# Kernel optimization log

Measured on AMD Instinct MI355X. Metric: run time of the kernel, lower is better.

## Reference

```python
import jax, jax.numpy as jnp
import numpy as np

B, C1, H, W = 2, 128, 64, 64
C_ = C1 // 2


def _conv2d(x, w, b, pad, dil):
    out = jax.lax.conv_general_dilated(
        x, w, (1, 1), [(pad, pad), (pad, pad)], rhs_dilation=(dil, dil),
        dimension_numbers=('NCHW', 'OIHW', 'NCHW'))
    return out + b[None, :, None, None]


def _deform_dw(x, off_w, off_b, w, k, pad, dil):
    # Depthwise DeformConv2d (v1, no modulation), offset_groups=1, stride=1.
    Bn, C, Hn, Wn = x.shape
    K = k * k
    offsets = _conv2d(x, off_w, off_b, pad, dil)          # [B, 2K, H, W]
    off = offsets.reshape(Bn, K, 2, Hn, Wn)               # (dy, dx) per kernel pt
    ky = jnp.repeat(jnp.arange(k) * dil, k).astype(x.dtype)   # [K]
    kx = jnp.tile(jnp.arange(k) * dil, k).astype(x.dtype)     # [K]
    py = off[:, :, 0] + (jnp.arange(Hn, dtype=x.dtype)[:, None] - pad) + ky[None, :, None, None]
    px = off[:, :, 1] + (jnp.arange(Wn, dtype=x.dtype)[None, :] - pad) + kx[None, :, None, None]
    y0 = jnp.floor(py); x0 = jnp.floor(px)
    ly = py - y0; lx = px - x0
    y0i = y0.astype(jnp.int32); x0i = x0.astype(jnp.int32)
    xf = x.reshape(Bn, C, Hn * Wn)

    def corner(yi, xi, wgt):
        valid = (yi >= 0) & (yi < Hn) & (xi >= 0) & (xi < Wn)
        idx = (jnp.clip(yi, 0, Hn - 1) * Wn + jnp.clip(xi, 0, Wn - 1)).reshape(Bn, -1)
        v = jax.vmap(lambda xb, ib: xb[:, ib])(xf, idx).reshape(Bn, C, K, Hn, Wn)
        return v * (wgt * valid.astype(x.dtype))[:, None]

    val = (corner(y0i, x0i, (1 - ly) * (1 - lx))
           + corner(y0i, x0i + 1, (1 - ly) * lx)
           + corner(y0i + 1, x0i, ly * (1 - lx))
           + corner(y0i + 1, x0i + 1, ly * lx))      # [B, C, K, H, W]
    return jnp.einsum('bckhw,ck->bchw', val, w.reshape(C, K))


def _forward(x, cv0_off_w, cv0_off_b, cv0_w, cvs_off_w, cvs_off_b, cvs_w,
             c0_off_w, c0_off_b, c0_w, cs_off_w, cs_off_b, cs_w,
             conv1_w, conv1_b, conv2_w, conv2_b):
    c = x.shape[1] // 2
    y0, y1 = x[:, :c], x[:, c:]
    a0 = _deform_dw(y0, cv0_off_w, cv0_off_b, cv0_w, 3, 1, 1)
    a0 = _deform_dw(a0, cvs_off_w, cvs_off_b, cvs_w, 5, 6, 3)
    a0 = _conv2d(a0, conv1_w, conv1_b, 0, 1)
    a1 = _deform_dw(y1, c0_off_w, c0_off_b, c0_w, 5, 2, 1)
    a1 = _deform_dw(a1, cs_off_w, cs_off_b, cs_w, 7, 9, 3)
    a1 = _conv2d(a1, conv2_w, conv2_b, 0, 1)
    return x * jnp.concatenate([a0, a1], axis=1)


def setup_inputs() -> dict:
    key = jax.random.key(0)
    ks = jax.random.split(key, 18)
    n = lambda k, sh, s: jax.random.normal(k, sh, dtype=jnp.float32) * s
    return {
        'x': n(ks[0], (B, C1, H, W), 1.0),
        'cv0_off_w': n(ks[1], (18, C_, 3, 3), 0.05),  'cv0_off_b': n(ks[2], (18,), 0.05),
        'cv0_w': n(ks[3], (C_, 1, 3, 3), 0.1),
        'cvs_off_w': n(ks[4], (50, C_, 5, 5), 0.05),  'cvs_off_b': n(ks[5], (50,), 0.05),
        'cvs_w': n(ks[6], (C_, 1, 5, 5), 0.1),
        'c0_off_w': n(ks[7], (50, C_, 5, 5), 0.05),   'c0_off_b': n(ks[8], (50,), 0.05),
        'c0_w': n(ks[9], (C_, 1, 5, 5), 0.1),
        'cs_off_w': n(ks[10], (98, C_, 7, 7), 0.05),  'cs_off_b': n(ks[11], (98,), 0.05),
        'cs_w': n(ks[12], (C_, 1, 7, 7), 0.1),
        'conv1_w': n(ks[13], (C_, C_, 1, 1), 0.1),    'conv1_b': n(ks[14], (C_,), 0.05),
        'conv2_w': n(ks[15], (C_, C_, 1, 1), 0.1),    'conv2_b': n(ks[16], (C_,), 0.05),
    }


def reference(x, cv0_off_w, cv0_off_b, cv0_w, cvs_off_w, cvs_off_b, cvs_w,
              c0_off_w, c0_off_b, c0_w, cs_off_w, cs_off_b, cs_w,
              conv1_w, conv1_b, conv2_w, conv2_b):
    return _forward(x, cv0_off_w, cv0_off_b, cv0_w, cvs_off_w, cvs_off_b, cvs_w,
                    c0_off_w, c0_off_b, c0_w, cs_off_w, cs_off_b, cs_w,
                    conv1_w, conv1_b, conv2_w, conv2_b)
```

## Files before the change

kernel.cpp:

```cpp
#include <hip/hip_runtime.h>
#include <hip/hip_bf16.h>

#define HW   4096

typedef __bf16 bf_t;
typedef __bf16 bf8_t __attribute__((ext_vector_type(8)));
typedef float  f4_t  __attribute__((ext_vector_type(4)));
typedef int    i4_t  __attribute__((ext_vector_type(4)));

#define OFF_A    0
#define OFF_B    409600
#define A1_F32   1212416
#define B1_F32   1736704
#define A2_F32   2260992
#define B2_F32   2785280
#define XA_F32   3309568
#define XB_F32   3833856
#define XA_HI    4358144
#define XA_LO    4620288
#define XB_HI    4882432
#define XB_LO    5144576
#define A1_HI    5406720
#define A1_LO    5668864
#define B1_HI    5931008
#define B1_LO    6193152
#define AW_A1    6455296
#define AW_B1    6464512
#define AW_A2    6515712
#define AW_B2    6566912
#define DW_A1    6767616
#define DW_B1    6768192
#define DW_A2    6769792
#define DW_B2    6771392
#define WS_TOT   6774528

__device__ __align__(16) float g_ws[WS_TOT];

__device__ __forceinline__ bf8_t bf8_zero() {
    bf8_t v;
#pragma unroll
    for (int j = 0; j < 8; ++j) v[j] = (bf_t)0.f;
    return v;
}

__device__ __forceinline__ void prep_wA_dev(const float* wg, int aw_off,
                                            int Cout, int K, int NCOT, int lb) {
    const int KK = K * K;
    const int total = KK * NCOT * 128;
    const int idx = lb * 256 + threadIdx.x;
    if (idx >= total) return;
    bf_t* aw = (bf_t*)(g_ws + aw_off);
    int lane = idx & 63;
    int kh   = (idx >> 6) & 1;
    int cot  = (idx >> 7) % NCOT;
    int tap  = idx / (128 * NCOT);
    int co   = cot * 16 + (lane & 15);
    int ci0  = kh * 32 + (lane >> 4) * 8;
    bf8_t v;
#pragma unroll
    for (int j = 0; j < 8; ++j) {
        float f = (co < Cout) ? wg[(co * 64 + ci0 + j) * KK + tap] : 0.f;
        v[j] = (bf_t)f;
    }
    *(bf8_t*)&aw[(long)idx * 8] = v;
}

__device__ __forceinline__ void prep_dwT_dev(const float* w, int dst_off,
                                             int KK, int lb) {
    const int idx = lb * 256 + threadIdx.x;
    if (idx < KK * 64) {
        int c = idx & 63, kk = idx >> 6;
        g_ws[dst_off + kk * 64 + c] = w[c * KK + kk];
    }
}

__global__ __launch_bounds__(256) void prep_split_kernel(
    const float* __restrict__ x,
    const float* cv0_off_w, const float* c0_off_w,
    const float* cvs_off_w, const float* cs_off_w,
    const float* cv0_w, const float* c0_w,
    const float* cvs_w, const float* cs_w)
{
    __shared__ float lds[16 * 68];
    const int bi = blockIdx.x;
    if (bi < 335) {
        if      (bi < 9)   prep_wA_dev(cv0_off_w, AW_A1, 18, 3, 2, bi);
        else if (bi < 59)  prep_wA_dev(c0_off_w,  AW_B1, 50, 5, 4, bi - 9);
        else if (bi < 109) prep_wA_dev(cvs_off_w, AW_A2, 50, 5, 4, bi - 59);
        else if (bi < 305) prep_wA_dev(cs_off_w,  AW_B2, 98, 7, 8, bi - 109);
        else if (bi < 308) prep_dwT_dev(cv0_w, DW_A1, 9,  bi - 305);
        else if (bi < 315) prep_dwT_dev(c0_w,  DW_B1, 25, bi - 308);
        else if (bi < 322) prep_dwT_dev(cvs_w, DW_A2, 25, bi - 315);
        else               prep_dwT_dev(cs_w,  DW_B2, 49, bi - 322);
        return;
    }
    const int s  = bi - 335;
    const int b  = s & 1;
    const int br = (s >> 1) & 1;
    const int p0 = (s >> 2) * 16;
    const float* sb = x + (long)b * (128 * HW) + (long)br * (64 * HW);
    bf_t*  dhi = (bf_t*)(g_ws + (br ? XB_HI : XA_HI));
    bf_t*  dlo = (bf_t*)(g_ws + (br ? XB_LO : XA_LO));
    float* df  = g_ws + (br ? XB_F32 : XA_F32);
    const int t = threadIdx.x;
    {
        const int px = t & 15;
        const int c0 = t >> 4;
#pragma unroll
        for (int pass = 0; pass < 4; ++pass) {
            int ci = c0 + pass * 16;
            lds[px * 68 + ci] = sb[ci * HW + p0 + px];
        }
    }
    __syncthreads();
    if (t < 128) {
        int px = t >> 3, q = t & 7;
        bf8_t vh, vl;
        f4_t  f0, f1;
#pragma unroll
        for (int j = 0; j < 8; ++j) {
            float a = lds[px * 68 + q * 8 + j];
            bf_t hcast = (bf_t)a;
            vh[j] = hcast;
            vl[j] = (bf_t)(a - (float)hcast);
            if (j < 4) f0[j] = a; else f1[j - 4] = a;
        }
        long base = (((long)b * 4096 + p0 + px) * 64) + q * 8;
        *(bf8_t*)&dhi[base] = vh;
        *(bf8_t*)&dlo[base] = vl;
        *(f4_t*)&df[base]     = f0;
        *(f4_t*)&df[base + 4] = f1;
    }
}

template<int K, int DIL, int PAD, int NCOT, int CPG>
__device__ __forceinline__ void mfma_conv_dev(
    int bx, int by, bf_t* smem,
    int hi_off, int lo_off, int aw_off, const float* __restrict__ bias,
    int dst_off, int Cout)
{
    constexpr int COLS = 64 + 2 * PAD;
    const bf_t* shi = (const bf_t*)(g_ws + hi_off);
    const bf_t* slo = (const bf_t*)(g_ws + lo_off);
    const bf_t* aw  = (const bf_t*)(g_ws + aw_off);
    float* dst = g_ws + dst_off;
    bf_t* lds0 = smem;
    bf_t* lds1 = smem + COLS * 72;

    const int t    = threadIdx.x;
    const int lane = t & 63;
    const int wv   = t >> 6;
    const int b    = bx >> 6;
    const int h    = bx & 63;
    const int ct0  = by * CPG;

    const int n0 = lane & 15;
    const int kq = lane >> 4;

    f4_t acc[CPG];
#pragma unroll
    for (int i = 0; i < CPG; ++i) acc[i] = (f4_t){0.f, 0.f, 0.f, 0.f};

    for (int ky = 0; ky < K; ++ky) {
        const int ih = h - PAD + ky * DIL;
        __syncthreads();
        if ((unsigned)ih < 64u) {
            const long rowb = ((long)b * 4096 + ih * 64) * 64;
            for (int c = t; c < COLS * 8; c += 256) {
                int col = c >> 3, q = c & 7;
                int iw = col - PAD;
                bf8_t vh, vl;
                if ((unsigned)iw < 64u) {
                    vh = *(const bf8_t*)&shi[rowb + iw * 64 + q * 8];
                    vl = *(const bf8_t*)&slo[rowb + iw * 64 + q * 8];
                } else { vh = bf8_zero(); vl = bf8_zero(); }
                *(bf8_t*)&lds0[col * 72 + q * 8] = vh;
                *(bf8_t*)&lds1[col * 72 + q * 8] = vl;
            }
        } else {
            bf8_t z = bf8_zero();
            for (int c = t; c < COLS * 8; c += 256) {
                int col = c >> 3, q = c & 7;
                *(bf8_t*)&lds0[col * 72 + q * 8] = z;
                *(bf8_t*)&lds1[col * 72 + q * 8] = z;
            }
        }
        __syncthreads();
#pragma unroll
        for (int kx = 0; kx < K; ++kx) {
            const int tap = ky * K + kx;
            bf8_t afr[CPG][2];
#pragma unroll
            for (int ct = 0; ct < CPG; ++ct)
#pragma unroll
                for (int kh = 0; kh < 2; ++kh)
                    afr[ct][kh] = *(const bf8_t*)
                        &aw[((((long)tap * NCOT + ct0 + ct) * 2 + kh) * 64 + lane) * 8];
            const int colb = (wv * 16 + n0 + kx * DIL) * 72;
#pragma unroll
            for (int kh = 0; kh < 2; ++kh) {
                const bf8_t bh = *(const bf8_t*)&lds0[colb + kh * 32 + kq * 8];
                const bf8_t bl = *(const bf8_t*)&lds1[colb + kh * 32 + kq * 8];
#pragma unroll
                for (int ct = 0; ct < CPG; ++ct) {
                    acc[ct] = __builtin_amdgcn_mfma_f32_16x16x32_bf16(
                        afr[ct][kh], bh, acc[ct], 0, 0, 0);
                    acc[ct] = __builtin_amdgcn_mfma_f32_16x16x32_bf16(
                        afr[ct][kh], bl, acc[ct], 0, 0, 0);
                }
            }
        }
    }

    const int w = wv * 16 + n0;
#pragma unroll
    for (int ct = 0; ct < CPG; ++ct) {
#pragma unroll
        for (int r = 0; r < 4; ++r) {
            int co = (ct0 + ct) * 16 + kq * 4 + r;
            if (co < Cout)
                dst[((long)b * Cout + co) * HW + h * 64 + w] = acc[ct][r] + bias[co];
        }
    }
}

__global__ __launch_bounds__(256) void conv_s1_kernel(
    const float* __restrict__ biasA, const float* __restrict__ biasB)
{
    extern __shared__ __align__(16) bf_t smem1[];
    const int bi = blockIdx.x;
    const int g = bi / 3, r = bi % 3;
    if (r == 0)
        mfma_conv_dev<3, 1, 1, 2, 1>(g & 127, g >> 7, smem1,
                                     XA_HI, XA_LO, AW_A1, biasA, OFF_A, 18);
    else {
        const int s = 2 * g + (r - 1);
        mfma_conv_dev<5, 1, 2, 4, 1>(s & 127, s >> 7, smem1,
                                     XB_HI, XB_LO, AW_B1, biasB, OFF_B, 50);
    }
}

__global__ __launch_bounds__(256) void conv_s2_kernel(
    const float* __restrict__ biasA, const float* __restrict__ biasB)
{
    extern __shared__ __align__(16) bf_t smem2[];
    const int bi = blockIdx.x;
    const int s = bi >> 1;
    if ((bi & 1) == 0)
        mfma_conv_dev<5, 3, 6, 4, 1>(s & 127, s >> 7, smem2,
                                     A1_HI, A1_LO, AW_A2, biasA, OFF_A, 50);
    else
        mfma_conv_dev<7, 3, 9, 8, 2>(s & 127, s >> 7, smem2,
                                     B1_HI, B1_LO, AW_B2, biasB, OFF_B, 98);
}

template<int KK, int WRITE_HILO>
__device__ __forceinline__ void sample_fused_dev(
    int bx, float* recs, int src_off, int off_off, int dwt_off,
    int dst_off, int hi_off, int lo_off, int K, int pad, int dil)
{
    const int t   = threadIdx.x;
    const int pgi = ((bx & 7) << 8) | (bx >> 3);

    for (int rec = t; rec < 4 * KK; rec += 256) {
        const int wv = rec & 3;
        const int kk = rec >> 2;
        const int pg = pgi * 4 + wv;
        const int b  = pg >> 12;
        const int p  = pg & 4095;
        const int h  = p >> 6, w = p & 63;
        const float oy = g_ws[off_off + ((long)(b * 2 * KK + 2 * kk)) * HW + p];
        const float ox = g_ws[off_off + ((long)(b * 2 * KK + 2 * kk + 1)) * HW + p];
        const float py = oy + (float)(h - pad + (kk / K) * dil);
        const float px = ox + (float)(w - pad + (kk % K) * dil);
        const float fy = floorf(py), fx = floorf(px);
        const float ly = py - fy,    lx = px - fx;
        const int y0 = (int)fy, x0 = (int)fx;
        const int y1 = y0 + 1,  x1 = x0 + 1;
        const float vy0 = ((unsigned)y0 < 64u) ? 1.f : 0.f;
        const float vy1 = ((unsigned)y1 < 64u) ? 1.f : 0.f;
        const float vx0 = ((unsigned)x0 < 64u) ? 1.f : 0.f;
        const float vx1 = ((unsigned)x1 < 64u) ? 1.f : 0.f;
        const float w00 = (1.f - ly) * (1.f - lx) * vy0 * vx0;
        const float w01 = (1.f - ly) * lx         * vy0 * vx1;
        const float w10 = ly         * (1.f - lx) * vy1 * vx0;
        const float w11 = ly         * lx         * vy1 * vx1;
        const int y0c = min(max(y0, 0), 63), y1c = min(max(y1, 0), 63);
        const int x0c = min(max(x0, 0), 63), x1c = min(max(x1, 0), 63);
        const int i00 = (y0c * 64 + x0c) * 256, i01 = (y0c * 64 + x1c) * 256;
        const int i10 = (y1c * 64 + x0c) * 256, i11 = (y1c * 64 + x1c) * 256;
        float* rp = &recs[rec * 8];
        *(f4_t*)rp       = (f4_t){w00, w01, w10, w11};
        *(i4_t*)(rp + 4) = (i4_t){i00, i01, i10, i11};
    }

    const int c  = t & 63;
    float wreg[KK];
    {
        const float* wtp = g_ws + dwt_off + c;
#pragma unroll
        for (int kk = 0; kk < KK; ++kk) wreg[kk] = wtp[kk * 64];
    }
    __syncthreads();

    const int wv = t >> 6;
    const int pg = pgi * 4 + wv;
    const int b  = pg >> 12;
    const int p  = pg & 4095;

    const char* sb = (const char*)(g_ws + src_off + ((long)b << 18)) + (c << 2);

    float acc = 0.f;
#pragma unroll
    for (int kk = 0; kk < KK; ++kk) {
        const float* rp = &recs[(kk * 4 + wv) * 8];
        const f4_t wq = *(const f4_t*)rp;
        const i4_t iq = *(const i4_t*)(rp + 4);
        const float v00 = *(const float*)(sb + iq.x);
        const float v01 = *(const float*)(sb + iq.y);
        const float v10 = *(const float*)(sb + iq.z);
        const float v11 = *(const float*)(sb + iq.w);
        const float val = wq.x * v00 + wq.y * v01 + wq.z * v10 + wq.w * v11;
        acc = fmaf(wreg[kk], val, acc);
    }

    const long ob = ((long)b * 4096 + p) * 64 + c;
    g_ws[dst_off + ob] = acc;
    if (WRITE_HILO) {
        bf_t h16 = (bf_t)acc;
        ((bf_t*)(g_ws + hi_off))[ob] = h16;
        ((bf_t*)(g_ws + lo_off))[ob] = (bf_t)(acc - (float)h16);
    }
}

template<int KA, int KB, int WRITE_HILO>
__global__ __launch_bounds__(256) void sample_kernel(
    int srcA, int offA, int dwtA, int dstA, int hiA, int loA, int padA, int dilA,
    int srcB, int offB, int dwtB, int dstB, int hiB, int loB, int padB, int dilB)
{
    __shared__ __align__(16) float recs[4 * 49 * 8];
    const int bx = blockIdx.x;
    const int s = bx >> 1;
    if ((bx & 1) == 0)
        sample_fused_dev<KA * KA, WRITE_HILO>(s, recs, srcA, offA, dwtA,
                                              dstA, hiA, loA, KA, padA, dilA);
    else
        sample_fused_dev<KB * KB, WRITE_HILO>(s, recs, srcB, offB, dwtB,
                                              dstB, hiB, loB, KB, padB, dilB);
}

__global__ __launch_bounds__(256) void final_kernel(
    const float* __restrict__ x,
    int aA_off, int aB_off,
    const float* __restrict__ w1, const float* __restrict__ b1,
    const float* __restrict__ w2, const float* __restrict__ b2,
    float* __restrict__ out)
{
    __shared__ float atile[64 * 65];
    __shared__ float wlds[64 * 32];
    const int t  = threadIdx.x;
    const int p0 = blockIdx.x * 64;
    const int by = blockIdx.y;
    const int b  = blockIdx.z;
    const bool brB  = (by >> 1) != 0;
    const int  cbase = (by & 1) * 32;
    const float* a  = g_ws + (brB ? aB_off : aA_off) + (long)b * (4096 * 64);
    const float* wg = brB ? w2 : w1;
    const float* bg = brB ? b2 : b1;

    {
        const int ci = t & 63;
        const int pxg = (t >> 6) * 16;
#pragma unroll
        for (int i = 0; i < 16; ++i) {
            int px = pxg + i;
            atile[px * 65 + ci] = a[(long)(p0 + px) * 64 + ci];
        }
    }
    for (int e = t; e < 2048; e += 256) {
        int col = e & 31, ci = e >> 5;
        wlds[ci * 32 + col] = wg[(cbase + col) * 64 + ci];
    }
    __syncthreads();

    const int px  = t & 63;
    const int cog = t >> 6;
    float acc[8] = {0, 0, 0, 0, 0, 0, 0, 0};
    for (int ci = 0; ci < 64; ++ci) {
        const float av = atile[px * 65 + ci];
        const float* wr = &wlds[ci * 32 + cog * 8];
#pragma unroll
        for (int j = 0; j < 8; ++j) acc[j] = fmaf(av, wr[j], acc[j]);
    }

    const int p = p0 + px;
#pragma unroll
    for (int j = 0; j < 8; ++j) {
        const int co = cbase + cog * 8 + j;
        const int cg = (brB ? 64 : 0) + co;
        const long o = ((long)b * 128 + cg) * HW + p;
        out[o] = (acc[j] + bg[co]) * x[o];
    }
}

extern "C" void kernel_launch(void* const* d_in, const int* in_sizes, int n_in,
                              void* d_out, int out_size, void* d_ws, size_t ws_size,
                              hipStream_t stream) {
    const float* x         = (const float*)d_in[0];
    const float* cv0_off_w = (const float*)d_in[1];
    const float* cv0_off_b = (const float*)d_in[2];
    const float* cv0_w     = (const float*)d_in[3];
    const float* cvs_off_w = (const float*)d_in[4];
    const float* cvs_off_b = (const float*)d_in[5];
    const float* cvs_w     = (const float*)d_in[6];
    const float* c0_off_w  = (const float*)d_in[7];
    const float* c0_off_b  = (const float*)d_in[8];
    const float* c0_w      = (const float*)d_in[9];
    const float* cs_off_w  = (const float*)d_in[10];
    const float* cs_off_b  = (const float*)d_in[11];
    const float* cs_w      = (const float*)d_in[12];
    const float* conv1_w   = (const float*)d_in[13];
    const float* conv1_b   = (const float*)d_in[14];
    const float* conv2_w   = (const float*)d_in[15];
    const float* conv2_b   = (const float*)d_in[16];
    float* out = (float*)d_out;
    (void)d_ws; (void)ws_size;

    prep_split_kernel<<<dim3(1359), 256, 0, stream>>>(
        x, cv0_off_w, c0_off_w, cvs_off_w, cs_off_w, cv0_w, c0_w, cvs_w, cs_w);

    conv_s1_kernel<<<dim3(768), 256, 19584, stream>>>(cv0_off_b, c0_off_b);

    sample_kernel<3, 5, 1><<<dim3(4096), 256, 0, stream>>>(
        XA_F32, OFF_A, DW_A1, A1_F32, A1_HI, A1_LO, 1, 1,
        XB_F32, OFF_B, DW_B1, B1_F32, B1_HI, B1_LO, 2, 1);

    conv_s2_kernel<<<dim3(1024), 256, 23616, stream>>>(cvs_off_b, cs_off_b);

    sample_kernel<5, 7, 0><<<dim3(4096), 256, 0, stream>>>(
        A1_F32, OFF_A, DW_A2, A2_F32, 0, 0, 6, 3,
        B1_F32, OFF_B, DW_B2, B2_F32, 0, 0, 9, 3);

    final_kernel<<<dim3(64, 4, 2), 256, 0, stream>>>(
        x, A2_F32, B2_F32, conv1_w, conv1_b, conv2_w, conv2_b, out);
}
```

Baseline: 201.3 us.

## Fuse final 1x1 conv and gating into second deformable sampling kernel

Removes the separate final kernel by doing the 1x1 pointwise conv, bias add and multiply by x inside the second sampling kernel. Each block stages its 4 pixels' 64-channel results in LDS and multiplies by a 64x64 weight matrix loaded into LDS. This avoids writing and re-reading the A2/B2 intermediates and saves a launch. In exchange, every block reloads the full weight matrix, LDS use per block rises, there is an extra barrier, and output stores are scattered across channels.

New measurement: 233.4 us. +15.9%, slower.

```diff
diff --git a/kernel.cpp b/kernel.cpp
--- a/kernel.cpp
+++ b/kernel.cpp
@@ -254,10 +254,13 @@
                                      B1_HI, B1_LO, AW_B2, biasB, OFF_B, 98);
 }
 
-template<int KK, int WRITE_HILO>
+template<int KK, int WRITE_HILO, int FUSE>
 __device__ __forceinline__ void sample_fused_dev(
-    int bx, float* recs, int src_off, int off_off, int dwt_off,
-    int dst_off, int hi_off, int lo_off, int K, int pad, int dil)
+    int bx, float* recs, float* wlds, float* a2t,
+    int src_off, int off_off, int dwt_off,
+    int dst_off, int hi_off, int lo_off, int K, int pad, int dil,
+    const float* __restrict__ xg, const float* __restrict__ wg,
+    const float* __restrict__ bg, float* __restrict__ outg, int brB)
 {
     const int t   = threadIdx.x;
     const int pgi = ((bx & 7) << 8) | (bx >> 3);
@@ -294,6 +297,13 @@
         *(i4_t*)(rp + 4) = (i4_t){i00, i01, i10, i11};
     }
 
+    if constexpr (FUSE) {
+        for (int e = t; e < 4096; e += 256) {
+            const int co = e & 63, ci = e >> 6;
+            wlds[ci * 64 + co] = wg[co * 64 + ci];
+        }
+    }
+
     const int c  = t & 63;
     float wreg[KK];
     {
@@ -324,83 +334,57 @@
         acc = fmaf(wreg[kk], val, acc);
     }
 
-    const long ob = ((long)b * 4096 + p) * 64 + c;
-    g_ws[dst_off + ob] = acc;
-    if (WRITE_HILO) {
-        bf_t h16 = (bf_t)acc;
-        ((bf_t*)(g_ws + hi_off))[ob] = h16;
-        ((bf_t*)(g_ws + lo_off))[ob] = (bf_t)(acc - (float)h16);
-    }
-}
-
-template<int KA, int KB, int WRITE_HILO>
+    if constexpr (!FUSE) {
+        const long ob = ((long)b * 4096 + p) * 64 + c;
+        g_ws[dst_off + ob] = acc;
+        if (WRITE_HILO) {
+            bf_t h16 = (bf_t)acc;
+            ((bf_t*)(g_ws + hi_off))[ob] = h16;
+            ((bf_t*)(g_ws + lo_off))[ob] = (bf_t)(acc - (float)h16);
+        }
+    } else {
+        a2t[wv * 68 + c] = acc;
+        __syncthreads();
+
+        const int co  = t & 63;
+        const int wv2 = t >> 6;
+        float acc2 = 0.f;
+        const float* arow = &a2t[wv2 * 68];
+#pragma unroll
+        for (int ci = 0; ci < 64; ++ci)
+            acc2 = fmaf(wlds[ci * 64 + co], arow[ci], acc2);
+
+        const int pg2 = pgi * 4 + wv2;
+        const int b2  = pg2 >> 12;
+        const int p2  = pg2 & 4095;
+        const int cg  = (brB ? 64 : 0) + co;
+        const long o  = ((long)b2 * 128 + cg) * (long)HW + p2;
+        outg[o] = (acc2 + bg[co]) * xg[o];
+    }
+}
+
+template<int KA, int KB, int WRITE_HILO, int FUSE>
 __global__ __launch_bounds__(256) void sample_kernel(
     int srcA, int offA, int dwtA, int dstA, int hiA, int loA, int padA, int dilA,
-    int srcB, int offB, int dwtB, int dstB, int hiB, int loB, int padB, int dilB)
+    int srcB, int offB, int dwtB, int dstB, int hiB, int loB, int padB, int dilB,
+    const float* __restrict__ xg,
+    const float* __restrict__ w1, const float* __restrict__ b1,
+    const float* __restrict__ w2, const float* __restrict__ b2,
+    float* __restrict__ outg)
 {
     __shared__ __align__(16) float recs[4 * 49 * 8];
+    __shared__ __align__(16) float wlds[FUSE ? 64 * 64 : 1];
+    __shared__ __align__(16) float a2t[FUSE ? 4 * 68 : 1];
     const int bx = blockIdx.x;
     const int s = bx >> 1;
     if ((bx & 1) == 0)
-        sample_fused_dev<KA * KA, WRITE_HILO>(s, recs, srcA, offA, dwtA,
-                                              dstA, hiA, loA, KA, padA, dilA);
+        sample_fused_dev<KA * KA, WRITE_HILO, FUSE>(s, recs, wlds, a2t,
+            srcA, offA, dwtA, dstA, hiA, loA, KA, padA, dilA,
+            xg, w1, b1, outg, 0);
     else
-        sample_fused_dev<KB * KB, WRITE_HILO>(s, recs, srcB, offB, dwtB,
-                                              dstB, hiB, loB, KB, padB, dilB);
-}
-
-__global__ __launch_bounds__(256) void final_kernel(
-    const float* __restrict__ x,
-    int aA_off, int aB_off,
-    const float* __restrict__ w1, const float* __restrict__ b1,
-    const float* __restrict__ w2, const float* __restrict__ b2,
-    float* __restrict__ out)
-{
-    __shared__ float atile[64 * 65];
-    __shared__ float wlds[64 * 32];
-    const int t  = threadIdx.x;
-    const int p0 = blockIdx.x * 64;
-    const int by = blockIdx.y;
-    const int b  = blockIdx.z;
-    const bool brB  = (by >> 1) != 0;
-    const int  cbase = (by & 1) * 32;
-    const float* a  = g_ws + (brB ? aB_off : aA_off) + (long)b * (4096 * 64);
-    const float* wg = brB ? w2 : w1;
-    const float* bg = brB ? b2 : b1;
-
-    {
-        const int ci = t & 63;
-        const int pxg = (t >> 6) * 16;
-#pragma unroll
-        for (int i = 0; i < 16; ++i) {
-            int px = pxg + i;
-            atile[px * 65 + ci] = a[(long)(p0 + px) * 64 + ci];
-        }
-    }
-    for (int e = t; e < 2048; e += 256) {
-        int col = e & 31, ci = e >> 5;
-        wlds[ci * 32 + col] = wg[(cbase + col) * 64 + ci];
-    }
-    __syncthreads();
-
-    const int px  = t & 63;
-    const int cog = t >> 6;
-    float acc[8] = {0, 0, 0, 0, 0, 0, 0, 0};
-    for (int ci = 0; ci < 64; ++ci) {
-        const float av = atile[px * 65 + ci];
-        const float* wr = &wlds[ci * 32 + cog * 8];
-#pragma unroll
-        for (int j = 0; j < 8; ++j) acc[j] = fmaf(av, wr[j], acc[j]);
-    }
-
-    const int p = p0 + px;
-#pragma unroll
-    for (int j = 0; j < 8; ++j) {
-        const int co = cbase + cog * 8 + j;
-        const int cg = (brB ? 64 : 0) + co;
-        const long o = ((long)b * 128 + cg) * HW + p;
-        out[o] = (acc[j] + bg[co]) * x[o];
-    }
+        sample_fused_dev<KB * KB, WRITE_HILO, FUSE>(s, recs, wlds, a2t,
+            srcB, offB, dwtB, dstB, hiB, loB, KB, padB, dilB,
+            xg, w2, b2, outg, 1);
 }
 
 extern "C" void kernel_launch(void* const* d_in, const int* in_sizes, int n_in,
@@ -431,16 +415,15 @@
 
     conv_s1_kernel<<<dim3(768), 256, 19584, stream>>>(cv0_off_b, c0_off_b);
 
-    sample_kernel<3, 5, 1><<<dim3(4096), 256, 0, stream>>>(
+    sample_kernel<3, 5, 1, 0><<<dim3(4096), 256, 0, stream>>>(
         XA_F32, OFF_A, DW_A1, A1_F32, A1_HI, A1_LO, 1, 1,
-        XB_F32, OFF_B, DW_B1, B1_F32, B1_HI, B1_LO, 2, 1);
+        XB_F32, OFF_B, DW_B1, B1_F32, B1_HI, B1_LO, 2, 1,
+        nullptr, nullptr, nullptr, nullptr, nullptr, nullptr);
 
     conv_s2_kernel<<<dim3(1024), 256, 23616, stream>>>(cvs_off_b, cs_off_b);
 
-    sample_kernel<5, 7, 0><<<dim3(4096), 256, 0, stream>>>(
+    sample_kernel<5, 7, 0, 1><<<dim3(4096), 256, 0, stream>>>(
         A1_F32, OFF_A, DW_A2, A2_F32, 0, 0, 6, 3,
-        B1_F32, OFF_B, DW_B2, B2_F32, 0, 0, 9, 3);
-
-    final_kernel<<<dim3(64, 4, 2), 256, 0, stream>>>(
-        x, A2_F32, B2_F32, conv1_w, conv1_b, conv2_w, conv2_b, out);
-}
+        B1_F32, OFF_B, DW_B2, B2_F32, 0, 0, 9, 3,
+        x, conv1_w, conv1_b, conv2_w, conv2_b, out);
+}
```

## Vectorize deformable sampling with float2 channel pairs and row-split bilinear halves

Applied to the files above, without the earlier changes.

Rewrites the deformable depthwise sampling inner loop so each lane handles two adjacent channels with float2 loads. Each wavefront is split into two halves, one per bilinear row, and the halves are combined with a cross-lane shuffle. Sample records now carry a clamped x base with remapped column weights, so each row needs only two contiguous reads. Depthwise weights are staged in LDS instead of per-thread registers. This halves per-lane gather instructions and register pressure, at the cost of a shuffle, idle lanes during the store, and extra LDS.

Result: slower. 228.2 us (+13.4%).

```diff
diff --git a/kernel.cpp b/kernel.cpp
--- a/kernel.cpp
+++ b/kernel.cpp
@@ -5,7 +5,9 @@
 
 typedef __bf16 bf_t;
 typedef __bf16 bf8_t __attribute__((ext_vector_type(8)));
+typedef __bf16 bf2_t __attribute__((ext_vector_type(2)));
 typedef float  f4_t  __attribute__((ext_vector_type(4)));
+typedef float  f2_t  __attribute__((ext_vector_type(2)));
 typedef int    i4_t  __attribute__((ext_vector_type(4)));
 
 #define OFF_A    0
@@ -256,7 +258,7 @@
 
 template<int KK, int WRITE_HILO>
 __device__ __forceinline__ void sample_fused_dev(
-    int bx, float* recs, int src_off, int off_off, int dwt_off,
+    int bx, float* recs, float* dwl, int src_off, int off_off, int dwt_off,
     int dst_off, int hi_off, int lo_off, int K, int pad, int dil)
 {
     const int t   = threadIdx.x;
@@ -277,59 +279,69 @@
         const float ly = py - fy,    lx = px - fx;
         const int y0 = (int)fy, x0 = (int)fx;
         const int y1 = y0 + 1,  x1 = x0 + 1;
-        const float vy0 = ((unsigned)y0 < 64u) ? 1.f : 0.f;
-        const float vy1 = ((unsigned)y1 < 64u) ? 1.f : 0.f;
-        const float vx0 = ((unsigned)x0 < 64u) ? 1.f : 0.f;
-        const float vx1 = ((unsigned)x1 < 64u) ? 1.f : 0.f;
-        const float w00 = (1.f - ly) * (1.f - lx) * vy0 * vx0;
-        const float w01 = (1.f - ly) * lx         * vy0 * vx1;
-        const float w10 = ly         * (1.f - lx) * vy1 * vx0;
-        const float w11 = ly         * lx         * vy1 * vx1;
+        const float ry0 = ((unsigned)y0 < 64u) ? (1.f - ly) : 0.f;
+        const float ry1 = ((unsigned)y1 < 64u) ? ly : 0.f;
+        const float cx0 = ((unsigned)x0 < 64u) ? (1.f - lx) : 0.f;
+        const float cx1 = ((unsigned)x1 < 64u) ? lx : 0.f;
+        const int xbase = min(max(x0, 0), 62);
+        const float sA = (xbase == x0) ? cx0 : ((xbase == x1) ? cx1 : 0.f);
+        const float sB = ((xbase + 1) == x1) ? cx1
+                                             : (((xbase + 1) == x0) ? cx0 : 0.f);
         const int y0c = min(max(y0, 0), 63), y1c = min(max(y1, 0), 63);
-        const int x0c = min(max(x0, 0), 63), x1c = min(max(x1, 0), 63);
-        const int i00 = (y0c * 64 + x0c) * 256, i01 = (y0c * 64 + x1c) * 256;
-        const int i10 = (y1c * 64 + x0c) * 256, i11 = (y1c * 64 + x1c) * 256;
+        const int a0 = (y0c * 64 + xbase) * 256;
+        const int a1 = (y1c * 64 + xbase) * 256;
         float* rp = &recs[rec * 8];
-        *(f4_t*)rp       = (f4_t){w00, w01, w10, w11};
-        *(i4_t*)(rp + 4) = (i4_t){i00, i01, i10, i11};
-    }
-
-    const int c  = t & 63;
-    float wreg[KK];
-    {
-        const float* wtp = g_ws + dwt_off + c;
-#pragma unroll
-        for (int kk = 0; kk < KK; ++kk) wreg[kk] = wtp[kk * 64];
-    }
+        f4_t r0, r1;
+        r0[0] = ry0 * sA; r0[1] = ry0 * sB;
+        r0[2] = __int_as_float(a0); r0[3] = 0.f;
+        r1[0] = ry1 * sA; r1[1] = ry1 * sB;
+        r1[2] = __int_as_float(a1); r1[3] = 0.f;
+        *(f4_t*)rp       = r0;
+        *(f4_t*)(rp + 4) = r1;
+    }
+
+    for (int e = t; e < KK * 64; e += 256) dwl[e] = g_ws[dwt_off + e];
     __syncthreads();
 
-    const int wv = t >> 6;
-    const int pg = pgi * 4 + wv;
-    const int b  = pg >> 12;
-    const int p  = pg & 4095;
-
-    const char* sb = (const char*)(g_ws + src_off + ((long)b << 18)) + (c << 2);
-
-    float acc = 0.f;
+    const int j    = t & 31;
+    const int half = (t >> 5) & 1;
+    const int wv   = t >> 6;
+    const int pg   = pgi * 4 + wv;
+    const int b    = pg >> 12;
+    const int p    = pg & 4095;
+
+    const char*  sb  = (const char*)(g_ws + src_off + ((long)b << 18)) + j * 8;
+    const float* dwp = dwl + 2 * j;
+
+    float ax = 0.f, ay = 0.f;
 #pragma unroll
     for (int kk = 0; kk < KK; ++kk) {
-        const float* rp = &recs[(kk * 4 + wv) * 8];
-        const f4_t wq = *(const f4_t*)rp;
-        const i4_t iq = *(const i4_t*)(rp + 4);
-        const float v00 = *(const float*)(sb + iq.x);
-        const float v01 = *(const float*)(sb + iq.y);
-        const float v10 = *(const float*)(sb + iq.z);
-        const float v11 = *(const float*)(sb + iq.w);
-        const float val = wq.x * v00 + wq.y * v01 + wq.z * v10 + wq.w * v11;
-        acc = fmaf(wreg[kk], val, acc);
-    }
-
-    const long ob = ((long)b * 4096 + p) * 64 + c;
-    g_ws[dst_off + ob] = acc;
-    if (WRITE_HILO) {
-        bf_t h16 = (bf_t)acc;
-        ((bf_t*)(g_ws + hi_off))[ob] = h16;
-        ((bf_t*)(g_ws + lo_off))[ob] = (bf_t)(acc - (float)h16);
+        const f4_t r = *(const f4_t*)&recs[(kk * 4 + wv) * 8 + half * 4];
+        const int addr = __float_as_int(r[2]);
+        const f2_t dw = *(const f2_t*)(dwp + kk * 64);
+        const char* rowp = sb + addr;
+        const f2_t vA = *(const f2_t*)rowp;
+        const f2_t vB = *(const f2_t*)(rowp + 256);
+        const float px0 = fmaf(r[0], vA[0], r[1] * vB[0]);
+        const float px1 = fmaf(r[0], vA[1], r[1] * vB[1]);
+        ax = fmaf(dw[0], px0, ax);
+        ay = fmaf(dw[1], px1, ay);
+    }
+
+    ax += __shfl_xor(ax, 32);
+    ay += __shfl_xor(ay, 32);
+
+    if (half == 0) {
+        const long ob = ((long)b * 4096 + p) * 64 + 2 * j;
+        f2_t o; o[0] = ax; o[1] = ay;
+        *(f2_t*)&g_ws[dst_off + ob] = o;
+        if (WRITE_HILO) {
+            bf_t hx = (bf_t)ax, hy = (bf_t)ay;
+            bf2_t h2; h2[0] = hx; h2[1] = hy;
+            bf2_t l2; l2[0] = (bf_t)(ax - (float)hx); l2[1] = (bf_t)(ay - (float)hy);
+            *(bf2_t*)&((bf_t*)(g_ws + hi_off))[ob] = h2;
+            *(bf2_t*)&((bf_t*)(g_ws + lo_off))[ob] = l2;
+        }
     }
 }
 
@@ -338,14 +350,16 @@
     int srcA, int offA, int dwtA, int dstA, int hiA, int loA, int padA, int dilA,
     int srcB, int offB, int dwtB, int dstB, int hiB, int loB, int padB, int dilB)
 {
-    __shared__ __align__(16) float recs[4 * 49 * 8];
+    constexpr int KKmax = KB * KB;
+    __shared__ __align__(16) float recs[4 * KKmax * 8];
+    __shared__ __align__(16) float dwl[KKmax * 64];
     const int bx = blockIdx.x;
     const int s = bx >> 1;
     if ((bx & 1) == 0)
-        sample_fused_dev<KA * KA, WRITE_HILO>(s, recs, srcA, offA, dwtA,
+        sample_fused_dev<KA * KA, WRITE_HILO>(s, recs, dwl, srcA, offA, dwtA,
                                               dstA, hiA, loA, KA, padA, dilA);
     else
-        sample_fused_dev<KB * KB, WRITE_HILO>(s, recs, srcB, offB, dwtB,
+        sample_fused_dev<KB * KB, WRITE_HILO>(s, recs, dwl, srcB, offB, dwtB,
                                               dstB, hiB, loB, KB, padB, dilB);
 }
 
```
